# Optimization experiments

Measured on AMD Instinct MI355X. Metric: run time of the kernel, lower is better.

The kernel has to match this reference:

```python
import jax, jax.numpy as jnp
import numpy as np

NEG_BIG = -1e10


def setup_inputs() -> dict:
    key = jax.random.key(0)
    k1, k2, k3 = jax.random.split(key, 3)
    B, C, S, H = 4, 32, 64, 256
    inputs = jax.random.normal(k1, (B, C, S, H), dtype=jnp.float32)
    mask = jnp.ones((B, C, S), dtype=jnp.float32)
    att_self = jax.random.uniform(k2, (B, C, S), dtype=jnp.float32)
    W = jax.random.normal(k3, (H, H), dtype=jnp.float32) * (1.0 / np.sqrt(H))
    return {"inputs": inputs, "mask": mask, "att_self": att_self, "W": W}


def reference(inputs, mask, att_self, W):
    # inputs: [B, C, S, H]; mask, att_self: [B, C, S]; W: [H, H] (linear1, no bias)
    # linear1(inputs2): x @ W^T applied to the query-side copy
    proj = jnp.einsum('bish,gh->bisg', inputs, W)          # [B, C, S, H]
    # scores[b,i,j,s,t] = proj[b,i,s,:] . inputs[b,j,t,:]
    scores = jnp.einsum('bish,bjth->bijst', proj, inputs)  # [B, C, C, S, S]
    # additive mask depends on (j, t) only (key side), broadcast over i and s
    scores = scores + (1.0 - mask)[:, None, :, None, :] * NEG_BIG
    # torch code computes softmax then overwrites with sigmoid -> sigmoid is effective
    att = jax.nn.sigmoid(scores)                            # [B, C, C, S, S]
    ctx = jnp.einsum('bijst,bjth->bijsh', att, inputs)      # [B, C, C, S, H]
    # selfatt weights over s (query sentence tokens), indexed by i
    fused = jnp.einsum('bis,bijsh->bijh', att_self, ctx)    # [B, C, C, H]
    return (fused, att)
```

## Files before the change

### kernel.cpp

```cpp
#include <hip/hip_runtime.h>
#include <hip/hip_bf16.h>

typedef __bf16 bf16x8 __attribute__((ext_vector_type(8)));
typedef float  f32x4  __attribute__((ext_vector_type(4)));

#define NEG_BIG (-1e10f)

constexpr int FUSED_N = 4 * 32 * 32 * 256;


__device__ __forceinline__ int swz16(int row, int g) {
    return (row * 16 + (g ^ (row & 15))) * 8;
}

__device__ __forceinline__ void stage_bf16(const __bf16* __restrict__ src,
                                           __bf16* sdst, int tid) {
#pragma unroll
    for (int it = 0; it < 4; ++it) {
        int idx = it * 256 + tid;
        int row = idx >> 4, gg = idx & 15;
        *(uint4*)&sdst[swz16(row, gg)] = *(const uint4*)&src[row * 256 + gg * 8];
    }
}

__device__ __forceinline__ void stage_cvt(const float* __restrict__ src,
                                          __bf16* sh, __bf16* sl, int tid) {
#pragma unroll
    for (int it = 0; it < 4; ++it) {
        int idx = it * 256 + tid;
        int row = idx >> 4, gg = idx & 15;
        const float* p = &src[row * 256 + gg * 8];
        float4 v0 = *(const float4*)p;
        float4 v1 = *(const float4*)(p + 4);
        float f[8] = {v0.x, v0.y, v0.z, v0.w, v1.x, v1.y, v1.z, v1.w};
        union { __bf16 b[8]; uint4 u; } H, L;
#pragma unroll
        for (int k = 0; k < 8; ++k) {
            __bf16 h = (__bf16)f[k];
            H.b[k] = h;
            L.b[k] = (__bf16)(f[k] - (float)h);
        }
        int o = swz16(row, gg);
        *(uint4*)&sh[o] = H.u;
        *(uint4*)&sl[o] = L.u;
    }
}

__device__ __forceinline__ void mfma3_chunk(const __bf16* sAh, const __bf16* sAl,
                                            const __bf16* sBh, const __bf16* sBl,
                                            int lane, int wave, f32x4 acc[4]) {
    const int m = lane & 15, quad = lane >> 4;
    const int arow = wave * 16 + m;
#pragma unroll
    for (int k0 = 0; k0 < 4; ++k0) {
        const int ag = k0 * 4 + quad;
        bf16x8 ah = *(const bf16x8*)&sAh[swz16(arow, ag)];
        bf16x8 al = *(const bf16x8*)&sAl[swz16(arow, ag)];
#pragma unroll
        for (int n = 0; n < 4; ++n) {
            const int bo = swz16(n * 16 + m, ag);
            bf16x8 bh = *(const bf16x8*)&sBh[bo];
            bf16x8 bl = *(const bf16x8*)&sBl[bo];
            acc[n] = __builtin_amdgcn_mfma_f32_16x16x32_bf16(ah, bh, acc[n], 0, 0, 0);
            acc[n] = __builtin_amdgcn_mfma_f32_16x16x32_bf16(ah, bl, acc[n], 0, 0, 0);
            acc[n] = __builtin_amdgcn_mfma_f32_16x16x32_bf16(al, bh, acc[n], 0, 0, 0);
        }
    }
}

__global__ __launch_bounds__(256) void convert_kernel(
    const float* __restrict__ src, __bf16* __restrict__ hi,
    __bf16* __restrict__ lo, int n4) {
    int i = blockIdx.x * 256 + threadIdx.x;
    if (i >= n4) return;
    float4 v = ((const float4*)src)[i];
    float f[4] = {v.x, v.y, v.z, v.w};
    union { __bf16 b[4]; uint2 u; } H, L;
#pragma unroll
    for (int k = 0; k < 4; ++k) {
        __bf16 h = (__bf16)f[k];
        H.b[k] = h;
        L.b[k] = (__bf16)(f[k] - (float)h);
    }
    *(uint2*)&hi[i * 4] = H.u;
    *(uint2*)&lo[i * 4] = L.u;
}

template <bool CVT>
__global__ __launch_bounds__(256, 2) void proj_kernel(
    const float* __restrict__ Xf, const float* __restrict__ Wf,
    const __bf16* __restrict__ Xh, const __bf16* __restrict__ Xl,
    const __bf16* __restrict__ Wh, const __bf16* __restrict__ Wl,
    __bf16* __restrict__ Ph, __bf16* __restrict__ Pl) {
    __shared__ __align__(16) __bf16 smem[4 * 64 * 128];
    __bf16* sAh = smem;
    __bf16* sAl = smem + 8192;
    __bf16* sBh = smem + 16384;
    __bf16* sBl = smem + 24576;
    const int tid = threadIdx.x;
    const int rb = blockIdx.x >> 2, gb = blockIdx.x & 3;
    const int lane = tid & 63, wave = tid >> 6;

    f32x4 acc[4];
    const f32x4 z = {0.f, 0.f, 0.f, 0.f};
#pragma unroll
    for (int n = 0; n < 4; ++n) acc[n] = z;

#pragma unroll
    for (int kc = 0; kc < 2; ++kc) {
        if (kc) __syncthreads();
        if (CVT) {
            stage_cvt(Xf + rb * 64 * 256 + kc * 128, sAh, sAl, tid);
            stage_cvt(Wf + gb * 64 * 256 + kc * 128, sBh, sBl, tid);
        } else {
            stage_bf16(Xh + rb * 64 * 256 + kc * 128, sAh, tid);
            stage_bf16(Xl + rb * 64 * 256 + kc * 128, sAl, tid);
            stage_bf16(Wh + gb * 64 * 256 + kc * 128, sBh, tid);
            stage_bf16(Wl + gb * 64 * 256 + kc * 128, sBl, tid);
        }
        __syncthreads();
        mfma3_chunk(sAh, sAl, sBh, sBl, lane, wave, acc);
    }

    const int m = lane & 15, quad = lane >> 4;
#pragma unroll
    for (int n = 0; n < 4; ++n)
#pragma unroll
        for (int r = 0; r < 4; ++r) {
            int row = rb * 64 + wave * 16 + quad * 4 + r;
            int col = gb * 64 + n * 16 + m;
            float v = acc[n][r];
            __bf16 h = (__bf16)v;
            Ph[row * 256 + col] = h;
            Pl[row * 256 + col] = (__bf16)(v - (float)h);
        }
}

template <bool CVT>
__global__ __launch_bounds__(256, 2) void main_kernel(
    const float* __restrict__ Xf, const float* __restrict__ maskf,
    const float* __restrict__ aselff,
    const __bf16* __restrict__ Xh, const __bf16* __restrict__ Xl,
    const __bf16* __restrict__ Ph, const __bf16* __restrict__ Pl,
    float* __restrict__ out) {
    __shared__ __align__(16) __bf16 smem[4 * 64 * 128];
    __bf16* sPh = smem;
    __bf16* sPl = smem + 8192;
    __bf16* sXh = smem + 16384;
    __bf16* sXl = smem + 24576;
    const int tid = threadIdx.x;
    const int j = blockIdx.x & 31;
    const int i = (blockIdx.x >> 5) & 31;
    const int b = blockIdx.x >> 10;
    const int lane = tid & 63, wave = tid >> 6;
    const int pr = (b * 32 + i) * 64 * 256;
    const int xr = (b * 32 + j) * 64 * 256;

    f32x4 acc[4];
    const f32x4 z = {0.f, 0.f, 0.f, 0.f};
#pragma unroll
    for (int n = 0; n < 4; ++n) acc[n] = z;

#pragma unroll
    for (int kc = 0; kc < 2; ++kc) {
        if (kc) __syncthreads();
        stage_bf16(Ph + pr + kc * 128, sPh, tid);
        stage_bf16(Pl + pr + kc * 128, sPl, tid);
        if (CVT) {
            stage_cvt(Xf + xr + kc * 128, sXh, sXl, tid);
        } else {
            stage_bf16(Xh + xr + kc * 128, sXh, tid);
            stage_bf16(Xl + xr + kc * 128, sXl, tid);
        }
        __syncthreads();
        mfma3_chunk(sPh, sPl, sXh, sXl, lane, wave, acc);
    }

    const int m = lane & 15, quad = lane >> 4;
    const float* mrow = maskf + (b * 32 + j) * 64;
    float att_v[16];
    float* outA = out + FUSED_N + ((b * 32 + i) * 32 + j) * 4096;
#pragma unroll
    for (int n = 0; n < 4; ++n) {
        const int t = n * 16 + m;
        const float madd = (1.0f - mrow[t]) * NEG_BIG;
#pragma unroll
        for (int r = 0; r < 4; ++r) {
            const int s = wave * 16 + quad * 4 + r;
            float x = acc[n][r] + madd;
            float a = 1.0f / (1.0f + __expf(-x));
            att_v[n * 4 + r] = a;
            outA[s * 64 + t] = a;
        }
    }

    __syncthreads();
    float* attS = (float*)smem;
#pragma unroll
    for (int n = 0; n < 4; ++n)
#pragma unroll
        for (int r = 0; r < 4; ++r)
            attS[(wave * 16 + quad * 4 + r) * 65 + (n * 16 + m)] = att_v[n * 4 + r];
    __syncthreads();

    float* s_w = attS + 64 * 65;
    if (tid < 64) {
        const float* arow = aselff + (b * 32 + i) * 64;
        float acw = 0.f;
        for (int s = 0; s < 64; ++s) acw += arow[s] * attS[s * 65 + tid];
        s_w[tid] = acw;
    }
    __syncthreads();

    const float* Xg = Xf + xr;
    float acf = 0.f;
#pragma unroll 8
    for (int t = 0; t < 64; ++t) acf += s_w[t] * Xg[t * 256 + tid];
    out[((b * 32 + i) * 32 + j) * 256 + tid] = acf;
}

extern "C" void kernel_launch(void* const* d_in, const int* in_sizes, int n_in,
                              void* d_out, int out_size, void* d_ws, size_t ws_size,
                              hipStream_t stream) {
    const float* X     = (const float*)d_in[0];
    const float* mask  = (const float*)d_in[1];
    const float* aself = (const float*)d_in[2];
    const float* W     = (const float*)d_in[3];
    float* out = (float*)d_out;

    __bf16* ws = (__bf16*)d_ws;
    const size_t NX = 2097152, NW = 65536;
    const size_t need_full = (4 * NX + 2 * NW) * sizeof(__bf16);

    if (ws_size >= need_full) {
        __bf16* Xh = ws;
        __bf16* Xl = Xh + NX;
        __bf16* Ph = Xl + NX;
        __bf16* Pl = Ph + NX;
        __bf16* Wh = Pl + NX;
        __bf16* Wl = Wh + NW;
        convert_kernel<<<dim3(2048), dim3(256), 0, stream>>>(X, Xh, Xl, (int)(NX / 4));
        convert_kernel<<<dim3(64), dim3(256), 0, stream>>>(W, Wh, Wl, (int)(NW / 4));
        proj_kernel<false><<<dim3(512), dim3(256), 0, stream>>>(
            X, W, Xh, Xl, Wh, Wl, Ph, Pl);
        main_kernel<false><<<dim3(4096), dim3(256), 0, stream>>>(
            X, mask, aself, Xh, Xl, Ph, Pl, out);
    } else {
        __bf16* Ph = ws;
        __bf16* Pl = Ph + NX;
        proj_kernel<true><<<dim3(512), dim3(256), 0, stream>>>(
            X, W, nullptr, nullptr, nullptr, nullptr, Ph, Pl);
        main_kernel<true><<<dim3(4096), dim3(256), 0, stream>>>(
            X, mask, aself, nullptr, nullptr, Ph, Pl, out);
    }
}
```

Before: 160.4 us.

## Fuse X conversion into projection, register-resident P tiles, two j per block

The X bf16 split conversion is merged into the projection kernel, which stages a full 64-row X tile in shared memory and reads W hi/lo directly from global. The main kernel keeps the query-side P fragments in registers across two j tiles per block, halving the grid. The selfatt weighting is now computed in registers with shuffle reductions instead of an LDS transpose. Launch bounds are raised for occupancy. The fallback path for small workspaces is removed, and the projection now runs on only 128 blocks, which may leave much of the GPU idle during that stage.

```diff
diff --git a/kernel.cpp b/kernel.cpp
--- a/kernel.cpp
+++ b/kernel.cpp
@@ -12,24 +12,40 @@
 __device__ __forceinline__ int swz16(int row, int g) {
     return (row * 16 + (g ^ (row & 15))) * 8;
 }
-
-__device__ __forceinline__ void stage_bf16(const __bf16* __restrict__ src,
-                                           __bf16* sdst, int tid) {
-#pragma unroll
-    for (int it = 0; it < 4; ++it) {
+__device__ __forceinline__ int swz32(int row, int g) {
+    return (row * 32 + (g ^ (row & 31))) * 8;
+}
+
+__global__ __launch_bounds__(256) void convw_kernel(
+    const float* __restrict__ W, __bf16* __restrict__ Wh, __bf16* __restrict__ Wl) {
+    int idx = blockIdx.x * 256 + threadIdx.x;
+    float4 v = ((const float4*)W)[idx];
+    float f[4] = {v.x, v.y, v.z, v.w};
+    union { __bf16 b[4]; uint2 u; } H, L;
+#pragma unroll
+    for (int k = 0; k < 4; ++k) {
+        __bf16 h = (__bf16)f[k];
+        H.b[k] = h;
+        L.b[k] = (__bf16)(f[k] - (float)h);
+    }
+    *(uint2*)&Wh[idx * 4] = H.u;
+    *(uint2*)&Wl[idx * 4] = L.u;
+}
+
+__global__ __launch_bounds__(256, 2) void prep_kernel(
+    const float* __restrict__ Xf,
+    const __bf16* __restrict__ Wh, const __bf16* __restrict__ Wl,
+    __bf16* __restrict__ XhG, __bf16* __restrict__ XlG,
+    __bf16* __restrict__ Ph, __bf16* __restrict__ Pl) {
+    __shared__ __align__(16) __bf16 sXh[64 * 256];
+    __shared__ __align__(16) __bf16 sXl[64 * 256];
+    const int tid = threadIdx.x, rb = blockIdx.x;
+    const float* src = Xf + rb * 64 * 256;
+#pragma unroll
+    for (int it = 0; it < 8; ++it) {
         int idx = it * 256 + tid;
-        int row = idx >> 4, gg = idx & 15;
-        *(uint4*)&sdst[swz16(row, gg)] = *(const uint4*)&src[row * 256 + gg * 8];
-    }
-}
-
-__device__ __forceinline__ void stage_cvt(const float* __restrict__ src,
-                                          __bf16* sh, __bf16* sl, int tid) {
-#pragma unroll
-    for (int it = 0; it < 4; ++it) {
-        int idx = it * 256 + tid;
-        int row = idx >> 4, gg = idx & 15;
-        const float* p = &src[row * 256 + gg * 8];
+        int row = idx >> 5, g = idx & 31;
+        const float* p = src + row * 256 + g * 8;
         float4 v0 = *(const float4*)p;
         float4 v1 = *(const float4*)(p + 4);
         float f[8] = {v0.x, v0.y, v0.z, v0.w, v1.x, v1.y, v1.z, v1.w};
@@ -40,183 +56,157 @@
             H.b[k] = h;
             L.b[k] = (__bf16)(f[k] - (float)h);
         }
-        int o = swz16(row, gg);
-        *(uint4*)&sh[o] = H.u;
-        *(uint4*)&sl[o] = L.u;
-    }
-}
-
-__device__ __forceinline__ void mfma3_chunk(const __bf16* sAh, const __bf16* sAl,
-                                            const __bf16* sBh, const __bf16* sBl,
-                                            int lane, int wave, f32x4 acc[4]) {
-    const int m = lane & 15, quad = lane >> 4;
+        int go = rb * 16384 + row * 256 + g * 8;
+        *(uint4*)&XhG[go] = H.u;
+        *(uint4*)&XlG[go] = L.u;
+        int o = swz32(row, g);
+        *(uint4*)&sXh[o] = H.u;
+        *(uint4*)&sXl[o] = L.u;
+    }
+    __syncthreads();
+
+    const int lane = tid & 63, wave = tid >> 6, m = lane & 15, quad = lane >> 4;
     const int arow = wave * 16 + m;
-#pragma unroll
-    for (int k0 = 0; k0 < 4; ++k0) {
-        const int ag = k0 * 4 + quad;
-        bf16x8 ah = *(const bf16x8*)&sAh[swz16(arow, ag)];
-        bf16x8 al = *(const bf16x8*)&sAl[swz16(arow, ag)];
-#pragma unroll
-        for (int n = 0; n < 4; ++n) {
-            const int bo = swz16(n * 16 + m, ag);
-            bf16x8 bh = *(const bf16x8*)&sBh[bo];
-            bf16x8 bl = *(const bf16x8*)&sBl[bo];
-            acc[n] = __builtin_amdgcn_mfma_f32_16x16x32_bf16(ah, bh, acc[n], 0, 0, 0);
-            acc[n] = __builtin_amdgcn_mfma_f32_16x16x32_bf16(ah, bl, acc[n], 0, 0, 0);
-            acc[n] = __builtin_amdgcn_mfma_f32_16x16x32_bf16(al, bh, acc[n], 0, 0, 0);
-        }
-    }
-}
-
-__global__ __launch_bounds__(256) void convert_kernel(
-    const float* __restrict__ src, __bf16* __restrict__ hi,
-    __bf16* __restrict__ lo, int n4) {
-    int i = blockIdx.x * 256 + threadIdx.x;
-    if (i >= n4) return;
-    float4 v = ((const float4*)src)[i];
-    float f[4] = {v.x, v.y, v.z, v.w};
-    union { __bf16 b[4]; uint2 u; } H, L;
-#pragma unroll
-    for (int k = 0; k < 4; ++k) {
-        __bf16 h = (__bf16)f[k];
-        H.b[k] = h;
-        L.b[k] = (__bf16)(f[k] - (float)h);
-    }
-    *(uint2*)&hi[i * 4] = H.u;
-    *(uint2*)&lo[i * 4] = L.u;
-}
-
-template <bool CVT>
-__global__ __launch_bounds__(256, 2) void proj_kernel(
-    const float* __restrict__ Xf, const float* __restrict__ Wf,
-    const __bf16* __restrict__ Xh, const __bf16* __restrict__ Xl,
-    const __bf16* __restrict__ Wh, const __bf16* __restrict__ Wl,
-    __bf16* __restrict__ Ph, __bf16* __restrict__ Pl) {
-    __shared__ __align__(16) __bf16 smem[4 * 64 * 128];
-    __bf16* sAh = smem;
-    __bf16* sAl = smem + 8192;
-    __bf16* sBh = smem + 16384;
-    __bf16* sBl = smem + 24576;
-    const int tid = threadIdx.x;
-    const int rb = blockIdx.x >> 2, gb = blockIdx.x & 3;
-    const int lane = tid & 63, wave = tid >> 6;
-
-    f32x4 acc[4];
+    bf16x8 Ah[8], Al[8];
+#pragma unroll
+    for (int k0 = 0; k0 < 8; ++k0) {
+        int o = swz32(arow, k0 * 4 + quad);
+        Ah[k0] = *(const bf16x8*)&sXh[o];
+        Al[k0] = *(const bf16x8*)&sXl[o];
+    }
     const f32x4 z = {0.f, 0.f, 0.f, 0.f};
 #pragma unroll
-    for (int n = 0; n < 4; ++n) acc[n] = z;
-
-#pragma unroll
-    for (int kc = 0; kc < 2; ++kc) {
-        if (kc) __syncthreads();
-        if (CVT) {
-            stage_cvt(Xf + rb * 64 * 256 + kc * 128, sAh, sAl, tid);
-            stage_cvt(Wf + gb * 64 * 256 + kc * 128, sBh, sBl, tid);
-        } else {
-            stage_bf16(Xh + rb * 64 * 256 + kc * 128, sAh, tid);
-            stage_bf16(Xl + rb * 64 * 256 + kc * 128, sAl, tid);
-            stage_bf16(Wh + gb * 64 * 256 + kc * 128, sBh, tid);
-            stage_bf16(Wl + gb * 64 * 256 + kc * 128, sBl, tid);
-        }
-        __syncthreads();
-        mfma3_chunk(sAh, sAl, sBh, sBl, lane, wave, acc);
-    }
-
-    const int m = lane & 15, quad = lane >> 4;
-#pragma unroll
-    for (int n = 0; n < 4; ++n)
-#pragma unroll
-        for (int r = 0; r < 4; ++r) {
-            int row = rb * 64 + wave * 16 + quad * 4 + r;
-            int col = gb * 64 + n * 16 + m;
-            float v = acc[n][r];
-            __bf16 h = (__bf16)v;
-            Ph[row * 256 + col] = h;
-            Pl[row * 256 + col] = (__bf16)(v - (float)h);
-        }
-}
-
-template <bool CVT>
-__global__ __launch_bounds__(256, 2) void main_kernel(
+    for (int ng = 0; ng < 4; ++ng) {
+        f32x4 acc[4];
+#pragma unroll
+        for (int n = 0; n < 4; ++n) acc[n] = z;
+#pragma unroll
+        for (int k0 = 0; k0 < 8; ++k0) {
+#pragma unroll
+            for (int n = 0; n < 4; ++n) {
+                int g = ng * 64 + n * 16 + m;
+                int wo = g * 256 + k0 * 32 + quad * 8;
+                bf16x8 bh = *(const bf16x8*)&Wh[wo];
+                bf16x8 bl = *(const bf16x8*)&Wl[wo];
+                acc[n] = __builtin_amdgcn_mfma_f32_16x16x32_bf16(Ah[k0], bh, acc[n], 0, 0, 0);
+                acc[n] = __builtin_amdgcn_mfma_f32_16x16x32_bf16(Ah[k0], bl, acc[n], 0, 0, 0);
+                acc[n] = __builtin_amdgcn_mfma_f32_16x16x32_bf16(Al[k0], bh, acc[n], 0, 0, 0);
+            }
+        }
+#pragma unroll
+        for (int n = 0; n < 4; ++n)
+#pragma unroll
+            for (int r = 0; r < 4; ++r) {
+                int row = rb * 64 + wave * 16 + quad * 4 + r;
+                int col = ng * 64 + n * 16 + m;
+                float v = acc[n][r];
+                __bf16 h = (__bf16)v;
+                Ph[row * 256 + col] = h;
+                Pl[row * 256 + col] = (__bf16)(v - (float)h);
+            }
+    }
+}
+
+__global__ __launch_bounds__(256, 4) void main_kernel(
     const float* __restrict__ Xf, const float* __restrict__ maskf,
     const float* __restrict__ aselff,
-    const __bf16* __restrict__ Xh, const __bf16* __restrict__ Xl,
+    const __bf16* __restrict__ XhG, const __bf16* __restrict__ XlG,
     const __bf16* __restrict__ Ph, const __bf16* __restrict__ Pl,
     float* __restrict__ out) {
-    __shared__ __align__(16) __bf16 smem[4 * 64 * 128];
-    __bf16* sPh = smem;
-    __bf16* sPl = smem + 8192;
-    __bf16* sXh = smem + 16384;
-    __bf16* sXl = smem + 24576;
+    __shared__ __align__(16) __bf16 sXh[64 * 128];
+    __shared__ __align__(16) __bf16 sXl[64 * 128];
+    __shared__ float sWpart[4 * 64];
+    __shared__ float s_w[64];
     const int tid = threadIdx.x;
-    const int j = blockIdx.x & 31;
-    const int i = (blockIdx.x >> 5) & 31;
-    const int b = blockIdx.x >> 10;
-    const int lane = tid & 63, wave = tid >> 6;
-    const int pr = (b * 32 + i) * 64 * 256;
-    const int xr = (b * 32 + j) * 64 * 256;
-
-    f32x4 acc[4];
+    const int jp = blockIdx.x & 15;
+    const int i = (blockIdx.x >> 4) & 31;
+    const int b = blockIdx.x >> 9;
+    const int lane = tid & 63, wave = tid >> 6, m = lane & 15, quad = lane >> 4;
+
+    const int prow = ((b * 32 + i) * 64 + wave * 16 + m) * 256;
+    bf16x8 Ah[8], Al[8];
+#pragma unroll
+    for (int k0 = 0; k0 < 8; ++k0) {
+        Ah[k0] = *(const bf16x8*)&Ph[prow + k0 * 32 + quad * 8];
+        Al[k0] = *(const bf16x8*)&Pl[prow + k0 * 32 + quad * 8];
+    }
+    const float4 aself4 = *(const float4*)&aselff[(b * 32 + i) * 64 + wave * 16 + quad * 4];
     const f32x4 z = {0.f, 0.f, 0.f, 0.f};
-#pragma unroll
-    for (int n = 0; n < 4; ++n) acc[n] = z;
-
-#pragma unroll
-    for (int kc = 0; kc < 2; ++kc) {
-        if (kc) __syncthreads();
-        stage_bf16(Ph + pr + kc * 128, sPh, tid);
-        stage_bf16(Pl + pr + kc * 128, sPl, tid);
-        if (CVT) {
-            stage_cvt(Xf + xr + kc * 128, sXh, sXl, tid);
-        } else {
-            stage_bf16(Xh + xr + kc * 128, sXh, tid);
-            stage_bf16(Xl + xr + kc * 128, sXl, tid);
+
+#pragma unroll
+    for (int jt = 0; jt < 2; ++jt) {
+        const int j = jp * 2 + jt;
+        const int xbase = (b * 32 + j) * 64 * 256;
+        f32x4 acc[4];
+#pragma unroll
+        for (int n = 0; n < 4; ++n) acc[n] = z;
+
+#pragma unroll
+        for (int kc = 0; kc < 2; ++kc) {
+            if (jt | kc) __syncthreads();
+#pragma unroll
+            for (int it = 0; it < 4; ++it) {
+                int idx = it * 256 + tid;
+                int row = idx >> 4, g = idx & 15;
+                int go = xbase + row * 256 + kc * 128 + g * 8;
+                int o = swz16(row, g);
+                *(uint4*)&sXh[o] = *(const uint4*)&XhG[go];
+                *(uint4*)&sXl[o] = *(const uint4*)&XlG[go];
+            }
+            __syncthreads();
+#pragma unroll
+            for (int k0 = 0; k0 < 4; ++k0) {
+                const int ak = kc * 4 + k0;
+#pragma unroll
+                for (int n = 0; n < 4; ++n) {
+                    int bo = swz16(n * 16 + m, k0 * 4 + quad);
+                    bf16x8 bh = *(const bf16x8*)&sXh[bo];
+                    bf16x8 bl = *(const bf16x8*)&sXl[bo];
+                    acc[n] = __builtin_amdgcn_mfma_f32_16x16x32_bf16(Ah[ak], bh, acc[n], 0, 0, 0);
+                    acc[n] = __builtin_amdgcn_mfma_f32_16x16x32_bf16(Ah[ak], bl, acc[n], 0, 0, 0);
+                    acc[n] = __builtin_amdgcn_mfma_f32_16x16x32_bf16(Al[ak], bh, acc[n], 0, 0, 0);
+                }
+            }
+        }
+
+        const float* mrow = maskf + (b * 32 + j) * 64;
+        float* outA = out + FUSED_N + ((size_t)((b * 32 + i) * 32 + j)) * 4096;
+        float part[4];
+#pragma unroll
+        for (int n = 0; n < 4; ++n) {
+            const int t = n * 16 + m;
+            const float madd = (1.0f - mrow[t]) * NEG_BIG;
+            float p = 0.f;
+#pragma unroll
+            for (int r = 0; r < 4; ++r) {
+                const int s = wave * 16 + quad * 4 + r;
+                float x = acc[n][r] + madd;
+                float a = 1.0f / (1.0f + __expf(-x));
+                outA[s * 64 + t] = a;
+                p += ((const float*)&aself4)[r] * a;
+            }
+            part[n] = p;
+        }
+#pragma unroll
+        for (int n = 0; n < 4; ++n) {
+            part[n] += __shfl_xor(part[n], 16, 64);
+            part[n] += __shfl_xor(part[n], 32, 64);
+        }
+        if (quad == 0) {
+#pragma unroll
+            for (int n = 0; n < 4; ++n) sWpart[wave * 64 + n * 16 + m] = part[n];
         }
         __syncthreads();
-        mfma3_chunk(sPh, sPl, sXh, sXl, lane, wave, acc);
-    }
-
-    const int m = lane & 15, quad = lane >> 4;
-    const float* mrow = maskf + (b * 32 + j) * 64;
-    float att_v[16];
-    float* outA = out + FUSED_N + ((b * 32 + i) * 32 + j) * 4096;
-#pragma unroll
-    for (int n = 0; n < 4; ++n) {
-        const int t = n * 16 + m;
-        const float madd = (1.0f - mrow[t]) * NEG_BIG;
-#pragma unroll
-        for (int r = 0; r < 4; ++r) {
-            const int s = wave * 16 + quad * 4 + r;
-            float x = acc[n][r] + madd;
-            float a = 1.0f / (1.0f + __expf(-x));
-            att_v[n * 4 + r] = a;
-            outA[s * 64 + t] = a;
-        }
-    }
-
-    __syncthreads();
-    float* attS = (float*)smem;
-#pragma unroll
-    for (int n = 0; n < 4; ++n)
-#pragma unroll
-        for (int r = 0; r < 4; ++r)
-            attS[(wave * 16 + quad * 4 + r) * 65 + (n * 16 + m)] = att_v[n * 4 + r];
-    __syncthreads();
-
-    float* s_w = attS + 64 * 65;
-    if (tid < 64) {
-        const float* arow = aselff + (b * 32 + i) * 64;
-        float acw = 0.f;
-        for (int s = 0; s < 64; ++s) acw += arow[s] * attS[s * 65 + tid];
-        s_w[tid] = acw;
-    }
-    __syncthreads();
-
-    const float* Xg = Xf + xr;
-    float acf = 0.f;
-#pragma unroll 8
-    for (int t = 0; t < 64; ++t) acf += s_w[t] * Xg[t * 256 + tid];
-    out[((b * 32 + i) * 32 + j) * 256 + tid] = acf;
+        if (tid < 64)
+            s_w[tid] = sWpart[tid] + sWpart[64 + tid] + sWpart[128 + tid] + sWpart[192 + tid];
+        __syncthreads();
+
+        const float* Xg = Xf + xbase;
+        float acf = 0.f;
+#pragma unroll
+        for (int t = 0; t < 64; ++t) acf += s_w[t] * Xg[t * 256 + tid];
+        out[((size_t)((b * 32 + i) * 32 + j)) * 256 + tid] = acf;
+    }
 }
 
 extern "C" void kernel_launch(void* const* d_in, const int* in_sizes, int n_in,
@@ -230,27 +220,15 @@
 
     __bf16* ws = (__bf16*)d_ws;
     const size_t NX = 2097152, NW = 65536;
-    const size_t need_full = (4 * NX + 2 * NW) * sizeof(__bf16);
-
-    if (ws_size >= need_full) {
-        __bf16* Xh = ws;
-        __bf16* Xl = Xh + NX;
-        __bf16* Ph = Xl + NX;
-        __bf16* Pl = Ph + NX;
-        __bf16* Wh = Pl + NX;
-        __bf16* Wl = Wh + NW;
-        convert_kernel<<<dim3(2048), dim3(256), 0, stream>>>(X, Xh, Xl, (int)(NX / 4));
-        convert_kernel<<<dim3(64), dim3(256), 0, stream>>>(W, Wh, Wl, (int)(NW / 4));
-        proj_kernel<false><<<dim3(512), dim3(256), 0, stream>>>(
-            X, W, Xh, Xl, Wh, Wl, Ph, Pl);
-        main_kernel<false><<<dim3(4096), dim3(256), 0, stream>>>(
-            X, mask, aself, Xh, Xl, Ph, Pl, out);
-    } else {
-        __bf16* Ph = ws;
-        __bf16* Pl = Ph + NX;
-        proj_kernel<true><<<dim3(512), dim3(256), 0, stream>>>(
-            X, W, nullptr, nullptr, nullptr, nullptr, Ph, Pl);
-        main_kernel<true><<<dim3(4096), dim3(256), 0, stream>>>(
-            X, mask, aself, nullptr, nullptr, Ph, Pl, out);
-    }
-}
+    __bf16* Xh = ws;
+    __bf16* Xl = Xh + NX;
+    __bf16* Ph = Xl + NX;
+    __bf16* Pl = Ph + NX;
+    __bf16* Wh = Pl + NX;
+    __bf16* Wl = Wh + NW;
+
+    convw_kernel<<<dim3(64), dim3(256), 0, stream>>>(W, Wh, Wl);
+    prep_kernel<<<dim3(128), dim3(256), 0, stream>>>(X, Wh, Wl, Xh, Xl, Ph, Pl);
+    main_kernel<<<dim3(2048), dim3(256), 0, stream>>>(
+        X, mask, aself, Xh, Xl, Ph, Pl, out);
+}
```

After: 195.5 us. 21.9% more time.
